# Kernel tuning notes

Hardware: AMD Instinct MI355X
Metric: run time of the kernel (lower is better)

The kernel has to match this reference:

```python
import jax, jax.numpy as jnp
import numpy as np

NUM_HEADS = 16
HEAD_DIM = 64  # hidden_size // num_heads = 1024 // 16


def setup_inputs() -> dict:
    key = jax.random.key(0)
    ks = jax.random.split(key, 5)
    B, S, D = 4, 2048, 1024
    scale = 1.0 / np.sqrt(D)
    return {
        "hidden_states": jax.random.normal(ks[0], (B, S, D), dtype=jnp.float32),
        "Wq": jax.random.normal(ks[1], (D, D), dtype=jnp.float32) * scale,
        "Wk": jax.random.normal(ks[2], (D, D), dtype=jnp.float32) * scale,
        "Wv": jax.random.normal(ks[3], (D, D), dtype=jnp.float32) * scale,
        "Wo": jax.random.normal(ks[4], (D, D), dtype=jnp.float32) * scale,
    }


def reference(hidden_states, Wq, Wk, Wv, Wo):
    B, S, D = hidden_states.shape
    H, hd = NUM_HEADS, HEAD_DIM
    # torch nn.Linear(y = x @ W.T), bias=False
    q = (hidden_states @ Wq.T).reshape(B, S, H, hd)
    k = (hidden_states @ Wk.T).reshape(B, S, H, hd)
    v = (hidden_states @ Wv.T).reshape(B, S, H, hd)
    q = q / jnp.sqrt(jnp.float32(hd))
    # scores: [B, H, S, S] — module materializes full score matrix
    scores = jnp.einsum("bqhd,bkhd->bhqk", q, k)
    weights = jax.nn.softmax(scores, axis=-1)
    attn = jnp.einsum("bhqk,bkhd->bqhd", weights, v).reshape(B, S, D)
    return attn @ Wo.T
```

## Files before the change

kernel.cpp:

```cpp
#include <hip/hip_runtime.h>

using u16 = unsigned short;
using u32 = unsigned int;
typedef __attribute__((ext_vector_type(8))) short bf16x8;
typedef __attribute__((ext_vector_type(4))) short bf16x4;
typedef __attribute__((ext_vector_type(4))) float f32x4;
typedef __attribute__((ext_vector_type(16))) float f32x16;
typedef __attribute__((ext_vector_type(4))) u32 u32x4;

__device__ __forceinline__ u16 f2bf(float f) {
  u32 u = __builtin_bit_cast(u32, f);
  u += 0x7FFFu + ((u >> 16) & 1u);
  return (u16)(u >> 16);
}

__device__ __forceinline__ void load_lds16(const void* g, void* l) {
  typedef const __attribute__((address_space(1))) u32 GA;
  typedef __attribute__((address_space(3))) u32 LA;
  __builtin_amdgcn_global_load_lds((GA*)g, (LA*)l, 16, 0, 0);
}

__device__ __forceinline__ bf16x4 tr16(const u16* p) {
  typedef __attribute__((address_space(3))) const u16 LT;
  bf16x4 d;
  asm volatile("ds_read_b64_tr_b16 %0, %1" : "=v"(d) : "v"((LT*)p));
  return d;
}

__device__ __forceinline__ float exp2_fast(float x) {
  float r;
  asm("v_exp_f32 %0, %1" : "=v"(r) : "v"(x));
  return r;
}

__device__ __forceinline__ u32 cvt_pk_bf16(float lo, float hi) {
  u32 r;
  asm("v_cvt_pk_bf16_f32 %0, %1, %2" : "=v"(r) : "v"(lo), "v"(hi));
  return r;
}

__device__ __forceinline__ void permlane32_swap(u32& a, u32& b) {
  asm volatile("v_permlane32_swap_b32 %0, %1" : "+v"(a), "+v"(b));
}

__global__ void cvt_bf16(const float* __restrict__ src, u16* __restrict__ dst,
                         int n4, float scale) {
  int i = blockIdx.x * blockDim.x + threadIdx.x;
  if (i >= n4) return;
  float4 v = reinterpret_cast<const float4*>(src)[i];
  ushort4 o;
  o.x = f2bf(v.x * scale);
  o.y = f2bf(v.y * scale);
  o.z = f2bf(v.z * scale);
  o.w = f2bf(v.w * scale);
  reinterpret_cast<ushort4*>(dst)[i] = o;
}

template <typename OutT>
__global__ __launch_bounds__(256, 2) void gemm_bt(
    const u16* __restrict__ A, const u16* __restrict__ Bw,
    OutT* __restrict__ C, int M, int N, int K) {
  __shared__ u16 At[128 * 32];
  __shared__ u16 Bt[128 * 32];
  const int tid = threadIdx.x;
  const int wid = tid >> 6, lane = tid & 63;
  const int wr = wid >> 1, wc = wid & 1;
  const int laneR = lane & 15, laneG = lane >> 4;
  const int laneK = laneG * 8;

  const int nbm = M >> 7;
  const int nwg = gridDim.x;
  const int cpx = nwg >> 3;
  const int id = blockIdx.x;
  const int swz = (id & 7) * cpx + (id >> 3);
  const int bm = swz % nbm, bn = swz / nbm;

  f32x4 acc[4][4];
#pragma unroll
  for (int i = 0; i < 4; ++i)
#pragma unroll
    for (int j = 0; j < 4; ++j) acc[i][j] = f32x4{0.f, 0.f, 0.f, 0.f};

  const int e0 = tid * 8;
  const int r0 = e0 >> 5, c0 = e0 & 31;
  const u16* Ab = A + (size_t)(bm * 128) * K;
  const u16* Bb = Bw + (size_t)(bn * 128) * K;

  for (int k0 = 0; k0 < K; k0 += 32) {
#pragma unroll
    for (int i = 0; i < 2; ++i) {
      load_lds16(Ab + (size_t)(i * 64 + r0) * K + k0 + c0, &At[(i * 256 + wid * 64) * 8]);
      load_lds16(Bb + (size_t)(i * 64 + r0) * K + k0 + c0, &Bt[(i * 256 + wid * 64) * 8]);
    }
    __syncthreads();
    bf16x8 af[4], bfr[4];
#pragma unroll
    for (int i = 0; i < 4; ++i)
      af[i] = *(const bf16x8*)&At[(wr * 64 + i * 16 + laneR) * 32 + laneK];
#pragma unroll
    for (int j = 0; j < 4; ++j)
      bfr[j] = *(const bf16x8*)&Bt[(wc * 64 + j * 16 + laneR) * 32 + laneK];
#pragma unroll
    for (int i = 0; i < 4; ++i)
#pragma unroll
      for (int j = 0; j < 4; ++j)
        acc[i][j] = __builtin_amdgcn_mfma_f32_16x16x32_bf16(af[i], bfr[j], acc[i][j], 0, 0, 0);
    __syncthreads();
  }

  const int crow = bm * 128 + wr * 64;
  const int ccol = bn * 128 + wc * 64;
#pragma unroll
  for (int i = 0; i < 4; ++i)
#pragma unroll
    for (int j = 0; j < 4; ++j)
#pragma unroll
      for (int r = 0; r < 4; ++r) {
        int row = crow + i * 16 + laneG * 4 + r;
        int col = ccol + j * 16 + laneR;
        float v = acc[i][j][r];
        if constexpr (sizeof(OutT) == 2)
          C[(size_t)row * N + col] = f2bf(v);
        else
          C[(size_t)row * N + col] = v;
      }
}

__global__ __launch_bounds__(512, 4) void flash_attn(
    const u16* __restrict__ QKV, u16* __restrict__ O) {
  constexpr int S = 2048, DQ = 3072, DO = 1024;
  __shared__ u16 Kt[2][4096];
  __shared__ u16 Vt[2][4096];
  const int tid = threadIdx.x, wid = tid >> 6, lane = tid & 63;
  const int lq = lane & 31, hi = lane >> 5;
  const int qt = blockIdx.x;
  const int b = blockIdx.y >> 4, h = blockIdx.y & 15;

  const size_t bq = (size_t)b * S * DQ;
  const u16* Qg = QKV + bq + h * 64;
  const u16* Kg = QKV + bq + 1024 + h * 64;
  const u16* Vg = QKV + bq + 2048 + h * 64;
  const int qrow0 = qt * 256 + wid * 32;

  const int k_kv = tid >> 3;
  const int k_col = ((tid & 7) ^ (k_kv & 7)) * 8;
  const int v_kv = ((tid >> 5) << 2) | ((tid >> 1) & 3);
  const int v_hd = (((tid >> 3) & 3) << 4) | ((tid & 1) << 3);

  bf16x8 qf[4];
#pragma unroll
  for (int kc = 0; kc < 4; ++kc)
    qf[kc] = *(const bf16x8*)&Qg[(size_t)(qrow0 + lq) * DQ + kc * 16 + hi * 8];

  f32x16 o0, o1;
#pragma unroll
  for (int r = 0; r < 16; ++r) { o0[r] = 0.f; o1[r] = 0.f; }
  float l = 0.f;

  auto stage = [&](int buf, int kv0) {
    load_lds16(Kg + (size_t)(kv0 + k_kv) * DQ + k_col, &Kt[buf][wid * 512]);
    load_lds16(Vg + (size_t)(kv0 + v_kv) * DQ + v_hd, &Vt[buf][wid * 512]);
  };

  stage(0, 0);
  __syncthreads();

  for (int t = 0; t < 32; ++t) {
    const int cur = t & 1;
    stage(cur ^ 1, ((t + 1) & 31) * 64);

    f32x16 st[2];
#pragma unroll
    for (int blk = 0; blk < 2; ++blk) {
#pragma unroll
      for (int r = 0; r < 16; ++r) st[blk][r] = 0.f;
      bf16x8 kf[4];
#pragma unroll
      for (int kc = 0; kc < 4; ++kc) {
        int kv = blk * 32 + lq;
        int byt = kv * 128 + ((kc * 32 + hi * 16) ^ ((kv & 7) << 4));
        kf[kc] = *(const bf16x8*)((const char*)&Kt[cur][0] + byt);
      }
      __builtin_amdgcn_s_setprio(1);
#pragma unroll
      for (int kc = 0; kc < 4; ++kc)
        st[blk] = __builtin_amdgcn_mfma_f32_32x32x16_bf16(kf[kc], qf[kc], st[blk], 0, 0, 0);
      __builtin_amdgcn_s_setprio(0);
    }

    float ps = 0.f;
#pragma unroll
    for (int blk = 0; blk < 2; ++blk)
#pragma unroll
      for (int r = 0; r < 16; ++r) {
        float p = exp2_fast(st[blk][r]);
        st[blk][r] = p;
        ps += p;
      }
    l += ps;

    u32 W0[8], W1[8];
#pragma unroll
    for (int r2 = 0; r2 < 8; ++r2) {
      W0[r2] = cvt_pk_bf16(st[0][2 * r2], st[0][2 * r2 + 1]);
      W1[r2] = cvt_pk_bf16(st[1][2 * r2], st[1][2 * r2 + 1]);
    }
    bf16x8 pb[4];
#pragma unroll
    for (int ks = 0; ks < 2; ++ks) {
      u32 a0 = W0[4 * ks], a2 = W0[4 * ks + 2];
      u32 a1 = W0[4 * ks + 1], a3 = W0[4 * ks + 3];
      permlane32_swap(a0, a2);
      permlane32_swap(a1, a3);
      pb[ks] = __builtin_bit_cast(bf16x8, u32x4{a0, a1, a2, a3});
    }
#pragma unroll
    for (int ks = 0; ks < 2; ++ks) {
      u32 a0 = W1[4 * ks], a2 = W1[4 * ks + 2];
      u32 a1 = W1[4 * ks + 1], a3 = W1[4 * ks + 3];
      permlane32_swap(a0, a2);
      permlane32_swap(a1, a3);
      pb[2 + ks] = __builtin_bit_cast(bf16x8, u32x4{a0, a1, a2, a3});
    }

#pragma unroll
    for (int c2 = 0; c2 < 2; ++c2) {
      bf16x4 vh[4][2];
      const int hb = c2 * 2 + ((lane >> 4) & 1);
#pragma unroll
      for (int ks = 0; ks < 4; ++ks)
#pragma unroll
        for (int p2 = 0; p2 < 2; ++p2) {
          int a = ks * 4 + hi * 2 + p2;
          vh[ks][p2] = tr16(&Vt[cur][(a * 4 + hb) * 64 + (lane & 15) * 4]);
        }
      asm volatile("s_waitcnt lgkmcnt(0)" ::: "memory");
      __builtin_amdgcn_sched_barrier(0);
      __builtin_amdgcn_s_setprio(1);
      f32x16 oc = c2 ? o1 : o0;
#pragma unroll
      for (int ks = 0; ks < 4; ++ks) {
        bf16x8 vf = __builtin_shufflevector(vh[ks][0], vh[ks][1], 0, 1, 2, 3, 4, 5, 6, 7);
        oc = __builtin_amdgcn_mfma_f32_32x32x16_bf16(vf, pb[ks], oc, 0, 0, 0);
      }
      if (c2) o1 = oc; else o0 = oc;
      __builtin_amdgcn_s_setprio(0);
    }

    __syncthreads();
  }

  l += __shfl_xor(l, 32);
  const float inv = 1.0f / l;
  const size_t boo = (size_t)b * S * DO + h * 64;
  const size_t qb = boo + (size_t)(qrow0 + lq) * DO;
#pragma unroll
  for (int r = 0; r < 16; ++r) {
    int hd = (r & 3) + 8 * (r >> 2) + 4 * hi;
    O[qb + hd] = f2bf(o0[r] * inv);
    O[qb + 32 + hd] = f2bf(o1[r] * inv);
  }
}

extern "C" void kernel_launch(void* const* d_in, const int* in_sizes, int n_in,
                              void* d_out, int out_size, void* d_ws, size_t ws_size,
                              hipStream_t stream) {
  const float* hs = (const float*)d_in[0];
  const float* Wq = (const float*)d_in[1];
  const float* Wk = (const float*)d_in[2];
  const float* Wv = (const float*)d_in[3];
  const float* Wo = (const float*)d_in[4];
  float* out = (float*)d_out;

  constexpr int Bn = 4, S = 2048, Dm = 1024;
  constexpr int M = Bn * S;
  constexpr size_t SZ = (size_t)M * Dm;
  constexpr size_t WSZ = (size_t)Dm * Dm;

  u16* wsp = (u16*)d_ws;
  u16* QKVb = wsp;
  u16* hs16 = QKVb + (size_t)M * 3072;
  u16* Ob = hs16;
  u16* W16 = hs16 + SZ;
  u16* Wo16 = W16 + 3 * WSZ;
  (void)ws_size; (void)in_sizes; (void)n_in; (void)out_size;

  cvt_bf16<<<(int)(SZ / 4 / 256), 256, 0, stream>>>(hs, hs16, (int)(SZ / 4), 1.0f);
  cvt_bf16<<<(int)(WSZ / 4 / 256), 256, 0, stream>>>(Wq, W16, (int)(WSZ / 4), 0.125f * 1.44269504f);
  cvt_bf16<<<(int)(WSZ / 4 / 256), 256, 0, stream>>>(Wk, W16 + WSZ, (int)(WSZ / 4), 1.0f);
  cvt_bf16<<<(int)(WSZ / 4 / 256), 256, 0, stream>>>(Wv, W16 + 2 * WSZ, (int)(WSZ / 4), 1.0f);
  cvt_bf16<<<(int)(WSZ / 4 / 256), 256, 0, stream>>>(Wo, Wo16, (int)(WSZ / 4), 1.0f);

  gemm_bt<u16><<<(M / 128) * (3072 / 128), 256, 0, stream>>>(hs16, W16, QKVb, M, 3072, Dm);

  flash_attn<<<dim3(S / 256, Bn * 16), 512, 0, stream>>>(QKVb, Ob);

  gemm_bt<float><<<(M / 128) * (Dm / 128), 256, 0, stream>>>(Ob, Wo16, out, M, Dm, Dm);
}
```

Before: 208.9 us.

## Rewrite GEMMs as pipelined 256x128 tiles, merge weight casts, swizzle attention grid

Measured after the change: 197.1 us. 1.06x faster.

```diff
diff --git a/kernel.cpp b/kernel.cpp
--- a/kernel.cpp
+++ b/kernel.cpp
@@ -56,24 +56,89 @@
   reinterpret_cast<ushort4*>(dst)[i] = o;
 }
 
+__global__ void cvt_w4(const float* __restrict__ Wq, const float* __restrict__ Wk,
+                       const float* __restrict__ Wv, const float* __restrict__ Wo,
+                       u16* __restrict__ dst, int n4seg, float qscale) {
+  int i = blockIdx.x * blockDim.x + threadIdx.x;
+  int seg = i / n4seg, off = i - seg * n4seg;
+  const float* src = seg == 0 ? Wq : seg == 1 ? Wk : seg == 2 ? Wv : Wo;
+  float sc = seg == 0 ? qscale : 1.0f;
+  float4 v = reinterpret_cast<const float4*>(src)[off];
+  ushort4 o;
+  o.x = f2bf(v.x * sc);
+  o.y = f2bf(v.y * sc);
+  o.z = f2bf(v.z * sc);
+  o.w = f2bf(v.w * sc);
+  reinterpret_cast<ushort4*>(dst)[i] = o;
+}
+
+template <int NH>
+__device__ __forceinline__ void mq(f32x4 (&acc)[4][4], bf16x8 (&afr)[4][2],
+                                   bf16x8 (&bfr)[2][2]) {
+  __builtin_amdgcn_s_setprio(1);
+#pragma unroll
+  for (int m = 0; m < 4; ++m)
+#pragma unroll
+    for (int n = 0; n < 2; ++n)
+#pragma unroll
+      for (int ks = 0; ks < 2; ++ks)
+        acc[m][NH * 2 + n] = __builtin_amdgcn_mfma_f32_16x16x32_bf16(
+            afr[m][ks], bfr[n][ks], acc[m][NH * 2 + n], 0, 0, 0);
+  __builtin_amdgcn_s_setprio(0);
+}
+
+#define GBAR() __builtin_amdgcn_s_barrier()
+#define PW()                                               \
+  do {                                                     \
+    GBAR();                                                \
+    asm volatile("s_waitcnt lgkmcnt(0)" ::: "memory");     \
+  } while (0)
+#define PWV(N)                                                          \
+  do {                                                                  \
+    GBAR();                                                             \
+    asm volatile("s_waitcnt vmcnt(" #N ") lgkmcnt(0)" ::: "memory");    \
+  } while (0)
+
 template <typename OutT>
-__global__ __launch_bounds__(256, 2) void gemm_bt(
+__global__ __launch_bounds__(512, 2) void gemm256x128(
     const u16* __restrict__ A, const u16* __restrict__ Bw,
     OutT* __restrict__ C, int M, int N, int K) {
-  __shared__ u16 At[128 * 32];
-  __shared__ u16 Bt[128 * 32];
+  __shared__ __align__(16) char ldsb[98304];
   const int tid = threadIdx.x;
   const int wid = tid >> 6, lane = tid & 63;
   const int wr = wid >> 1, wc = wid & 1;
   const int laneR = lane & 15, laneG = lane >> 4;
-  const int laneK = laneG * 8;
-
-  const int nbm = M >> 7;
-  const int nwg = gridDim.x;
-  const int cpx = nwg >> 3;
+  const int swzR = (laneR & 7) << 4;
+
+  const int nbm = M >> 8;
+  const int cpx = gridDim.x >> 3;
   const int id = blockIdx.x;
-  const int swz = (id & 7) * cpx + (id >> 3);
-  const int bm = swz % nbm, bn = swz / nbm;
+  const int swzid = (id & 7) * cpx + (id >> 3);
+  const int bm = swzid % nbm, bn = swzid / nbm;
+
+  const u16* Ab = A + (size_t)(bm * 256) * K;
+  const u16* Bb = Bw + (size_t)(bn * 128) * K;
+
+  const int s_r = tid >> 3;
+  const int s_k = ((tid & 7) ^ (s_r & 7)) * 8;
+
+  auto stage_unit = [&](const u16* Xb, int dstoff, int row0, int kt) {
+    char* d = ldsb + dstoff + wid * 1024;
+#pragma unroll
+    for (int j = 0; j < 2; ++j)
+      load_lds16(Xb + (size_t)(row0 + j * 64 + s_r) * K + kt * 64 + s_k,
+                 d + j * 8192);
+  };
+  auto rdA = [&](int buf, int m, int ks) -> bf16x8 {
+    return *(const bf16x8*)(ldsb + buf * 32768 + (wr >> 1) * 16384 +
+                            ((wr & 1) * 64 + m * 16 + laneR) * 128 +
+                            ((ks * 64 + laneG * 16) ^ swzR));
+  };
+  auto rdB = [&](int buf, int nh, int n, int ks) -> bf16x8 {
+    return *(const bf16x8*)(ldsb + 65536 + buf * 16384 +
+                            (wc * 64 + nh * 32 + n * 16 + laneR) * 128 +
+                            ((ks * 64 + laneG * 16) ^ swzR));
+  };
 
   f32x4 acc[4][4];
 #pragma unroll
@@ -81,44 +146,66 @@
 #pragma unroll
     for (int j = 0; j < 4; ++j) acc[i][j] = f32x4{0.f, 0.f, 0.f, 0.f};
 
-  const int e0 = tid * 8;
-  const int r0 = e0 >> 5, c0 = e0 & 31;
-  const u16* Ab = A + (size_t)(bm * 128) * K;
-  const u16* Bb = Bw + (size_t)(bn * 128) * K;
-
-  for (int k0 = 0; k0 < K; k0 += 32) {
-#pragma unroll
-    for (int i = 0; i < 2; ++i) {
-      load_lds16(Ab + (size_t)(i * 64 + r0) * K + k0 + c0, &At[(i * 256 + wid * 64) * 8]);
-      load_lds16(Bb + (size_t)(i * 64 + r0) * K + k0 + c0, &Bt[(i * 256 + wid * 64) * 8]);
-    }
-    __syncthreads();
-    bf16x8 af[4], bfr[4];
-#pragma unroll
-    for (int i = 0; i < 4; ++i)
-      af[i] = *(const bf16x8*)&At[(wr * 64 + i * 16 + laneR) * 32 + laneK];
-#pragma unroll
-    for (int j = 0; j < 4; ++j)
-      bfr[j] = *(const bf16x8*)&Bt[(wc * 64 + j * 16 + laneR) * 32 + laneK];
-#pragma unroll
-    for (int i = 0; i < 4; ++i)
-#pragma unroll
-      for (int j = 0; j < 4; ++j)
-        acc[i][j] = __builtin_amdgcn_mfma_f32_16x16x32_bf16(af[i], bfr[j], acc[i][j], 0, 0, 0);
-    __syncthreads();
+  bf16x8 afr[4][2], bfr[2][2];
+  auto readA = [&](int buf) {
+#pragma unroll
+    for (int m = 0; m < 4; ++m) {
+      afr[m][0] = rdA(buf, m, 0);
+      afr[m][1] = rdA(buf, m, 1);
+    }
+  };
+  auto readB = [&](int buf, int nh) {
+#pragma unroll
+    for (int n = 0; n < 2; ++n) {
+      bfr[n][0] = rdB(buf, nh, n, 0);
+      bfr[n][1] = rdB(buf, nh, n, 1);
+    }
+  };
+
+  const int NT = K >> 6, NI = K >> 7;
+
+  stage_unit(Ab, 0, 0, 0);
+  stage_unit(Ab, 16384, 128, 0);
+  stage_unit(Bb, 65536, 0, 0);
+  stage_unit(Ab, 32768, 0, 1);
+  asm volatile("s_waitcnt vmcnt(2)" ::: "memory");
+  GBAR();
+
+  for (int i = 0; i < NI; ++i) {
+    const int tb = (2 * i + 1) & (NT - 1);
+    const int tc = (2 * i + 2) & (NT - 1);
+    const int td = (2 * i + 3) & (NT - 1);
+    readA(0); readB(0, 0);
+    stage_unit(Ab, 32768 + 16384, 128, tb);
+    stage_unit(Bb, 65536 + 16384, 0, tb);
+    PW();
+    mq<0>(acc, afr, bfr); GBAR();
+    readB(0, 1);
+    stage_unit(Ab, 0, 0, tc);
+    stage_unit(Ab, 16384, 128, tc);
+    PWV(4);
+    mq<1>(acc, afr, bfr); GBAR();
+    readA(1); readB(1, 0);
+    stage_unit(Bb, 65536, 0, tc);
+    PW();
+    mq<0>(acc, afr, bfr); GBAR();
+    readB(1, 1);
+    stage_unit(Ab, 32768, 0, td);
+    PWV(2);
+    mq<1>(acc, afr, bfr); GBAR();
   }
 
-  const int crow = bm * 128 + wr * 64;
+  const int crow = bm * 256 + wr * 64;
   const int ccol = bn * 128 + wc * 64;
 #pragma unroll
-  for (int i = 0; i < 4; ++i)
-#pragma unroll
-    for (int j = 0; j < 4; ++j)
+  for (int mf = 0; mf < 4; ++mf)
+#pragma unroll
+    for (int nf = 0; nf < 4; ++nf)
 #pragma unroll
       for (int r = 0; r < 4; ++r) {
-        int row = crow + i * 16 + laneG * 4 + r;
-        int col = ccol + j * 16 + laneR;
-        float v = acc[i][j][r];
+        int row = crow + mf * 16 + laneG * 4 + r;
+        int col = ccol + nf * 16 + laneR;
+        float v = acc[mf][nf][r];
         if constexpr (sizeof(OutT) == 2)
           C[(size_t)row * N + col] = f2bf(v);
         else
@@ -133,8 +220,11 @@
   __shared__ u16 Vt[2][4096];
   const int tid = threadIdx.x, wid = tid >> 6, lane = tid & 63;
   const int lq = lane & 31, hi = lane >> 5;
-  const int qt = blockIdx.x;
-  const int b = blockIdx.y >> 4, h = blockIdx.y & 15;
+
+  const int id = blockIdx.x;
+  const int jj0 = id >> 3;
+  const int bh = (id & 7) * 8 + (jj0 >> 3), qt = jj0 & 7;
+  const int b = bh >> 4, h = bh & 15;
 
   const size_t bq = (size_t)b * S * DQ;
   const u16* Qg = QKV + bq + h * 64;
@@ -286,14 +376,12 @@
   (void)ws_size; (void)in_sizes; (void)n_in; (void)out_size;
 
   cvt_bf16<<<(int)(SZ / 4 / 256), 256, 0, stream>>>(hs, hs16, (int)(SZ / 4), 1.0f);
-  cvt_bf16<<<(int)(WSZ / 4 / 256), 256, 0, stream>>>(Wq, W16, (int)(WSZ / 4), 0.125f * 1.44269504f);
-  cvt_bf16<<<(int)(WSZ / 4 / 256), 256, 0, stream>>>(Wk, W16 + WSZ, (int)(WSZ / 4), 1.0f);
-  cvt_bf16<<<(int)(WSZ / 4 / 256), 256, 0, stream>>>(Wv, W16 + 2 * WSZ, (int)(WSZ / 4), 1.0f);
-  cvt_bf16<<<(int)(WSZ / 4 / 256), 256, 0, stream>>>(Wo, Wo16, (int)(WSZ / 4), 1.0f);
-
-  gemm_bt<u16><<<(M / 128) * (3072 / 128), 256, 0, stream>>>(hs16, W16, QKVb, M, 3072, Dm);
-
-  flash_attn<<<dim3(S / 256, Bn * 16), 512, 0, stream>>>(QKVb, Ob);
-
-  gemm_bt<float><<<(M / 128) * (Dm / 128), 256, 0, stream>>>(Ob, Wo16, out, M, Dm, Dm);
-}
+  cvt_w4<<<(int)(4 * WSZ / 4 / 256), 256, 0, stream>>>(
+      Wq, Wk, Wv, Wo, W16, (int)(WSZ / 4), 0.125f * 1.44269504f);
+
+  gemm256x128<u16><<<(M / 256) * (3072 / 128), 512, 0, stream>>>(hs16, W16, QKVb, M, 3072, Dm);
+
+  flash_attn<<<512, 512, 0, stream>>>(QKVb, Ob);
+
+  gemm256x128<float><<<(M / 256) * (Dm / 128), 512, 0, stream>>>(Ob, Wo16, out, M, Dm, Dm);
+}
```
